# Kernel optimization log

Measured on AMD Instinct MI355X. Metric: run time of the kernel, lower is better.

Reference implementation:

```python
import jax, jax.numpy as jnp
import numpy as np

N = 600000          # points
V = 120000          # occupied voxels (60k per sample)
BEV_H = 512
BEV_W = 512
B = 2
BN_EPS = 1e-3


def setup_inputs() -> dict:
    key = jax.random.key(0)
    k1, k2, k3, k4, k5 = jax.random.split(key, 5)
    bev_coordinate = jax.random.normal(k1, (N, 3), jnp.float32) * 20.0
    bev_local_coordinate = jax.random.normal(k2, (N, 3), jnp.float32)
    intensity = jax.random.uniform(k3, (N,), jnp.float32)
    bev_mapping_pv = jax.random.randint(k4, (N,), 0, V, jnp.int32)
    # unique (batch, h, w) per voxel: 60k voxels/sample spread over 512*512 grid
    v = np.arange(V)
    per_batch = V // B
    flat = (v % per_batch) * (BEV_H * BEV_W // per_batch)  # stride 4, unique
    bev_mapping_vf = jnp.asarray(
        np.stack([v // per_batch, flat // BEV_W, flat % BEV_W], axis=1),
        dtype=jnp.int32)
    W = jax.random.normal(k5, (64, 10), jnp.float32) * (1.0 / np.sqrt(10))
    gamma = jnp.ones((64,), jnp.float32)
    beta = jnp.zeros((64,), jnp.float32)
    return {
        "bev_coordinate": bev_coordinate,
        "bev_local_coordinate": bev_local_coordinate,
        "intensity": intensity,
        "bev_mapping_pv": bev_mapping_pv,
        "bev_mapping_vf": bev_mapping_vf,
        "W": W,
        "gamma": gamma,
        "beta": beta,
        "batch_size": B,
    }


def reference(bev_coordinate, bev_local_coordinate, intensity,
              bev_mapping_pv, bev_mapping_vf, W, gamma, beta, batch_size):
    nvox = bev_mapping_vf.shape[0]
    pv = bev_mapping_pv
    # scatterMean: per-voxel mean of coordinates, gathered back per point
    counts = jnp.zeros((nvox,), bev_coordinate.dtype).at[pv].add(1.0)
    sums = jnp.zeros((nvox, 3), bev_coordinate.dtype).at[pv].add(bev_coordinate)
    vox_mean = sums / jnp.maximum(counts, 1.0)[:, None]
    point_mean = vox_mean[pv]                              # [N,3]
    # feature: [coord(3), intensity(1), coord-mean(3), local(3)] -> [N,10]
    feature = jnp.concatenate(
        [bev_coordinate, intensity[:, None],
         bev_coordinate - point_mean, bev_local_coordinate], axis=1)
    # Linear(10,64,bias=False) + BatchNorm1d(train mode, batch stats) + ReLU
    x = feature @ W.T                                      # [N,64]
    mu = jnp.mean(x, axis=0)
    var = jnp.mean(jnp.square(x - mu), axis=0)             # biased, as torch BN
    x = (x - mu) * jax.lax.rsqrt(var + BN_EPS) * gamma + beta
    x = jax.nn.relu(x)
    # scatterMax into voxels, empty voxels stay at finfo.min (as torch impl)
    vox_max = jnp.full((nvox, 64), jnp.finfo(x.dtype).min, x.dtype).at[pv].max(x)
    # dense scatter_nd into [B,H,W,64], then channels_first
    dense = jnp.zeros((batch_size, BEV_H, BEV_W, 64), x.dtype)
    dense = dense.at[bev_mapping_vf[:, 0], bev_mapping_vf[:, 1],
                     bev_mapping_vf[:, 2]].set(vox_max)
    return jnp.transpose(dense, (0, 3, 1, 2))              # [B,64,H,W]
```

## Files before the change

### kernel.cpp

```cpp
#include <hip/hip_runtime.h>
#include <float.h>

#define EMPTY_FILL (-3.3895313892515355e38f)

#define HW 262144
#define BEVW 512
#define NBPM 256



__global__ void k_init(int* counts, int V, int* inv, int ncell) {
    int i = blockIdx.x * blockDim.x + threadIdx.x;
    int st = gridDim.x * blockDim.x;
    for (int t = i; t < V; t += st) counts[t] = 0;
    for (int t = i; t < ncell; t += st) inv[t] = -1;
}

__global__ void k_count(const int* __restrict__ pv, int n, int* __restrict__ counts) {
    int i = blockIdx.x * blockDim.x + threadIdx.x;
    if (i < n) atomicAdd(&counts[pv[i]], 1);
}

__global__ void k_scan1(const int* __restrict__ counts, int V, int* __restrict__ partials) {
    __shared__ int sh[256];
    int base = blockIdx.x * 2048;
    int s = 0;
    for (int e = 0; e < 8; ++e) {
        int idx = base + e * 256 + threadIdx.x;
        if (idx < V) s += counts[idx];
    }
    sh[threadIdx.x] = s; __syncthreads();
    for (int d = 128; d > 0; d >>= 1) {
        if (threadIdx.x < d) sh[threadIdx.x] += sh[threadIdx.x + d];
        __syncthreads();
    }
    if (threadIdx.x == 0) partials[blockIdx.x] = sh[0];
}

__global__ void k_scan2(const int* __restrict__ partials, int NB, int* __restrict__ blockoff) {
    __shared__ int sh[256];
    int run = 0;
    for (int base = 0; base < NB; base += 256) {
        int idx = base + threadIdx.x;
        int p = (idx < NB) ? partials[idx] : 0;
        __syncthreads();
        sh[threadIdx.x] = p; __syncthreads();
        for (int d = 1; d < 256; d <<= 1) {
            int v2 = sh[threadIdx.x];
            if (threadIdx.x >= d) v2 += sh[threadIdx.x - d];
            __syncthreads(); sh[threadIdx.x] = v2; __syncthreads();
        }
        if (idx < NB) blockoff[idx] = run + sh[threadIdx.x] - p;
        run += sh[255];
    }
}

__global__ void k_scan3(const int* __restrict__ counts, int V,
                        const int* __restrict__ blockoff, int* __restrict__ cursor) {
    __shared__ int sh[256];
    int t = threadIdx.x;
    int base = blockIdx.x * 2048 + t * 8;
    int c[8]; int s = 0;
#pragma unroll
    for (int e = 0; e < 8; ++e) {
        int idx = base + e;
        c[e] = (idx < V) ? counts[idx] : 0;
        s += c[e];
    }
    sh[t] = s; __syncthreads();
    for (int d = 1; d < 256; d <<= 1) {
        int v2 = sh[t];
        if (t >= d) v2 += sh[t - d];
        __syncthreads(); sh[t] = v2; __syncthreads();
    }
    int run = blockoff[blockIdx.x] + sh[t] - s;
#pragma unroll
    for (int e = 0; e < 8; ++e) {
        int idx = base + e;
        if (idx < V) cursor[idx] = run;
        run += c[e];
    }
}

__global__ void k_fill(const int* __restrict__ pv,
                       const float* __restrict__ coord,
                       const float* __restrict__ locc,
                       const float* __restrict__ inten, int n,
                       int* __restrict__ cursor,
                       float4* __restrict__ pdata) {
    int i = blockIdx.x * blockDim.x + threadIdx.x;
    if (i >= n) return;
    int pos = atomicAdd(&cursor[pv[i]], 1);
    pdata[2*pos]   = make_float4(coord[3*i], coord[3*i+1], coord[3*i+2], inten[i]);
    pdata[2*pos+1] = make_float4(locc[3*i],  locc[3*i+1],  locc[3*i+2],  0.f);
}

__global__ void k_pmoments(const float* __restrict__ coord,
                           const float* __restrict__ locc,
                           const float* __restrict__ inten, int n,
                           float* __restrict__ parts) {
    __shared__ float sm[35];
    if (threadIdx.x < 35) sm[threadIdx.x] = 0.f;
    __syncthreads();
    float acc[35];
#pragma unroll
    for (int t = 0; t < 35; ++t) acc[t] = 0.f;
    int i = blockIdx.x * blockDim.x + threadIdx.x;
    int st = gridDim.x * blockDim.x;
    for (; i < n; i += st) {
        float r[7];
        r[0] = coord[3*i]; r[1] = coord[3*i+1]; r[2] = coord[3*i+2];
        r[3] = inten[i];
        r[4] = locc[3*i]; r[5] = locc[3*i+1]; r[6] = locc[3*i+2];
        int t = 0;
#pragma unroll
        for (int j = 0; j < 7; ++j)
#pragma unroll
            for (int k = j; k < 7; ++k) { acc[t] += r[j]*r[k]; ++t; }
#pragma unroll
        for (int j = 0; j < 7; ++j) acc[28+j] += r[j];
    }
#pragma unroll
    for (int t = 0; t < 35; ++t) {
        float x = acc[t];
#pragma unroll
        for (int m = 1; m < 64; m <<= 1) x += __shfl_xor(x, m, 64);
        acc[t] = x;
    }
    if ((threadIdx.x & 63) == 0) {
#pragma unroll
        for (int t = 0; t < 35; ++t) atomicAdd(&sm[t], acc[t]);
    }
    __syncthreads();
    if (threadIdx.x < 35) parts[blockIdx.x * 35 + threadIdx.x] = sm[threadIdx.x];
}

__global__ void k_voxstat(const float4* __restrict__ pdata,
                          const int* __restrict__ counts,
                          const int* __restrict__ cursor, int V,
                          float* __restrict__ vmean,
                          float* __restrict__ parts) {
    __shared__ float sm[18];
    if (threadIdx.x < 18) sm[threadIdx.x] = 0.f;
    __syncthreads();
    int v = blockIdx.x * blockDim.x + threadIdx.x;
    float acc[18];
#pragma unroll
    for (int t = 0; t < 18; ++t) acc[t] = 0.f;
    if (v < V) {
        int cnt = counts[v];
        int end = cursor[v];
        int st = end - cnt;
        float s0=0.f,s1=0.f,s2=0.f,si=0.f,l0=0.f,l1=0.f,l2=0.f;
        for (int k = st; k < end; ++k) {
            float4 a = pdata[2*k];
            float4 b = pdata[2*k+1];
            s0 += a.x; s1 += a.y; s2 += a.z; si += a.w;
            l0 += b.x; l1 += b.y; l2 += b.z;
        }
        float inv_ = 1.f / fmaxf((float)cnt, 1.f);
        float m0 = s0*inv_, m1 = s1*inv_, m2 = s2*inv_;
        vmean[3*v] = m0; vmean[3*v+1] = m1; vmean[3*v+2] = m2;
        float cf = (float)cnt;
        acc[0]=cf*m0*m0; acc[1]=cf*m0*m1; acc[2]=cf*m0*m2;
        acc[3]=cf*m1*m1; acc[4]=cf*m1*m2; acc[5]=cf*m2*m2;
        acc[6]=m0*si; acc[7]=m1*si; acc[8]=m2*si;
        acc[9]=m0*l0;  acc[10]=m0*l1; acc[11]=m0*l2;
        acc[12]=m1*l0; acc[13]=m1*l1; acc[14]=m1*l2;
        acc[15]=m2*l0; acc[16]=m2*l1; acc[17]=m2*l2;
    }
#pragma unroll
    for (int t = 0; t < 18; ++t) {
        float x = acc[t];
#pragma unroll
        for (int m = 1; m < 64; m <<= 1) x += __shfl_xor(x, m, 64);
        acc[t] = x;
    }
    if ((threadIdx.x & 63) == 0) {
#pragma unroll
        for (int t = 0; t < 18; ++t) atomicAdd(&sm[t], acc[t]);
    }
    __syncthreads();
    if (threadIdx.x < 18) parts[blockIdx.x * 18 + threadIdx.x] = sm[threadIdx.x];
}

__global__ void k_bn_final(const float* __restrict__ pm, int nbpm,
                           const float* __restrict__ pvs, int nbvs,
                           const float* __restrict__ W,
                           const float* __restrict__ gamma,
                           const float* __restrict__ beta,
                           int n, float* __restrict__ ss) {
    __shared__ double red[53][16];
    __shared__ double g[53];
    __shared__ double MF[10][10];
    __shared__ double SF[10];
    int tid = threadIdx.x;
    int t16 = tid >> 4;
    int l16 = tid & 15;
    double s = 0.0;
    if (t16 < 35) {
        for (int b = l16; b < nbpm; b += 16) s += (double)pm[b * 35 + t16];
        red[t16][l16] = s;
    } else if (t16 < 53) {
        int u = t16 - 35;
        for (int b = l16; b < nbvs; b += 16) s += (double)pvs[b * 18 + u];
        red[t16][l16] = s;
    }
    __syncthreads();
    if (tid < 53) {
        double a = 0.0;
#pragma unroll
        for (int k = 0; k < 16; ++k) a += red[tid][k];
        g[tid] = a;
    }
    __syncthreads();
    if (tid == 0) {
        double M7[7][7], S7[7], Pmm[3][3], Qmi[3], Rml[3][3];
        int t = 0;
        for (int j = 0; j < 7; ++j)
            for (int k = j; k < 7; ++k) { M7[j][k] = M7[k][j] = g[t]; ++t; }
        for (int j = 0; j < 7; ++j) S7[j] = g[28+j];
        t = 35;
        for (int j = 0; j < 3; ++j)
            for (int k = j; k < 3; ++k) { Pmm[j][k] = Pmm[k][j] = g[t]; ++t; }
        for (int k = 0; k < 3; ++k) Qmi[k] = g[41+k];
        for (int j = 0; j < 3; ++j)
            for (int k = 0; k < 3; ++k) Rml[j][k] = g[44+3*j+k];
        const int rmap[10] = {0,1,2,3,-1,-1,-1,4,5,6};
        for (int a = 0; a < 10; ++a)
            for (int b = a; b < 10; ++b) {
                bool ad = (a >= 4 && a < 7), bd = (b >= 4 && b < 7);
                double val;
                if (!ad && !bd) val = M7[rmap[a]][rmap[b]];
                else if (ad && bd) val = M7[a-4][b-4] - Pmm[a-4][b-4];
                else {
                    int k = ad ? a-4 : b-4;
                    int o = ad ? b : a;
                    int ro = rmap[o];
                    double X;
                    if (o < 3) X = Pmm[o][k];
                    else if (o == 3) X = Qmi[k];
                    else X = Rml[k][ro-4];
                    val = M7[ro][k] - X;
                }
                MF[a][b] = MF[b][a] = val;
            }
        for (int a = 0; a < 10; ++a)
            SF[a] = (a >= 4 && a < 7) ? 0.0 : S7[rmap[a]];
    }
    __syncthreads();
    int c = tid;
    if (c >= 64) return;
    double w[10];
    for (int j = 0; j < 10; ++j) w[j] = (double)W[c*10+j];
    double invn = 1.0 / (double)n;
    double mu = 0.0;
    for (int j = 0; j < 10; ++j) mu += w[j] * SF[j] * invn;
    double ex2 = 0.0;
    for (int j = 0; j < 10; ++j) {
        double sj = 0.0;
        for (int k = 0; k < 10; ++k) sj += MF[j][k] * w[k];
        ex2 += w[j] * sj;
    }
    ex2 *= invn;
    double var = ex2 - mu*mu;
    double scale = (double)gamma[c] / sqrt(var + 1e-3);
    double shift = (double)beta[c] - mu*scale;
    ss[c] = (float)scale;
    ss[64+c] = (float)shift;
}

__global__ void k_vox(const float4* __restrict__ pdata,
                      const int* __restrict__ counts,
                      const int* __restrict__ cursor,
                      const float* __restrict__ vmean,
                      const int* __restrict__ vf, int V,
                      const float* __restrict__ W,
                      const float* __restrict__ ss,
                      float* __restrict__ vfeat,
                      int* __restrict__ inv) {
    const int lane = threadIdx.x & 63;
    const int wave = blockIdx.x * (blockDim.x >> 6) + (threadIdx.x >> 6);
    const int nw = gridDim.x * (blockDim.x >> 6);
    const int vpw = (V + nw - 1) / nw;
    const int v0 = wave * vpw;
    if (v0 >= V) return;
    const int v1 = (v0 + vpw < V) ? (v0 + vpw) : V;
    float wr[10];
#pragma unroll
    for (int j = 0; j < 10; ++j) wr[j] = W[lane*10 + j];
    const float scale = ss[lane];
    const float shift = ss[64 + lane];
    const float su0 = (wr[0]+wr[4])*scale, su1 = (wr[1]+wr[5])*scale,
                su2 = (wr[2]+wr[6])*scale, sw3 = wr[3]*scale,
                sw7 = wr[7]*scale, sw8 = wr[8]*scale, sw9 = wr[9]*scale,
                sv0 = wr[4]*scale, sv1 = wr[5]*scale, sv2 = wr[6]*scale;
    for (int v = v0; v < v1; ++v) {
        const int cnt = counts[v];
        const int end = cursor[v];
        float m;
        if (cnt == 0) {
            m = EMPTY_FILL;
        } else {
            const float off = shift - (sv0*vmean[3*v] + sv1*vmean[3*v+1]
                                       + sv2*vmean[3*v+2]);
            float mm = -FLT_MAX;
#pragma unroll 2
            for (int k = end - cnt; k < end; ++k) {
                float4 a = pdata[2*k];
                float4 b = pdata[2*k+1];
                float y = su0*a.x + su1*a.y + su2*a.z + sw3*a.w
                        + sw7*b.x + sw8*b.y + sw9*b.z;
                mm = fmaxf(mm, y);
            }
            m = fmaxf(mm + off, 0.f);
        }
        vfeat[(size_t)v*64 + lane] = m;
        if (lane == 0) {
            inv[vf[3*v]*HW + vf[3*v+1]*BEVW + vf[3*v+2]] = v;
        }
    }
}

__global__ void k_out(const float* __restrict__ vfeat,
                      const int* __restrict__ inv,
                      int ncell, float* __restrict__ out) {
    int cell = blockIdx.x * blockDim.x + threadIdx.x;
    if (cell >= ncell) return;
    int v = inv[cell];
    int b = cell >> 18;
    int hw = cell & (HW - 1);
    float* ob = out + ((size_t)b << 24) + hw;
    const float4* vb = (const float4*)(vfeat + (size_t)(v >= 0 ? v : 0) * 64);
#pragma unroll
    for (int c0 = 0; c0 < 16; ++c0) {
        float4 q = (v >= 0) ? vb[c0] : make_float4(0.f, 0.f, 0.f, 0.f);
        ob[(size_t)(4*c0+0) * HW] = q.x;
        ob[(size_t)(4*c0+1) * HW] = q.y;
        ob[(size_t)(4*c0+2) * HW] = q.z;
        ob[(size_t)(4*c0+3) * HW] = q.w;
    }
}


__global__ void k_zero4(float4* a, long na, float4* b, long nb) {
    long i = (long)blockIdx.x * blockDim.x + threadIdx.x;
    long st = (long)gridDim.x * blockDim.x;
    float4 z = make_float4(0.f, 0.f, 0.f, 0.f);
    for (long t = i; t < na; t += st) a[t] = z;
    for (long t = i; t < nb; t += st) b[t] = z;
}

__global__ void k_scatter_mean7(const float* __restrict__ coord,
                                const float* __restrict__ locc,
                                const float* __restrict__ inten,
                                const int* __restrict__ pv, int n,
                                float* __restrict__ countsf,
                                float* __restrict__ sums7) {
    int i = blockIdx.x * blockDim.x + threadIdx.x;
    if (i >= n) return;
    int v = pv[i];
    atomicAdd(&countsf[v], 1.0f);
    atomicAdd(&sums7[7*v+0], coord[3*i+0]);
    atomicAdd(&sums7[7*v+1], coord[3*i+1]);
    atomicAdd(&sums7[7*v+2], coord[3*i+2]);
    atomicAdd(&sums7[7*v+3], inten[i]);
    atomicAdd(&sums7[7*v+4], locc[3*i+0]);
    atomicAdd(&sums7[7*v+5], locc[3*i+1]);
    atomicAdd(&sums7[7*v+6], locc[3*i+2]);
}

__global__ void k_vstat_fb(const float* __restrict__ countsf,
                           const float* __restrict__ sums7, int V,
                           float* __restrict__ vmean, float* __restrict__ parts) {
    __shared__ float sm[18];
    if (threadIdx.x < 18) sm[threadIdx.x] = 0.f;
    __syncthreads();
    int v = blockIdx.x * blockDim.x + threadIdx.x;
    float acc[18];
#pragma unroll
    for (int t = 0; t < 18; ++t) acc[t] = 0.f;
    if (v < V) {
        float cf = countsf[v];
        float inv_ = 1.f / fmaxf(cf, 1.f);
        float m0 = sums7[7*v]*inv_, m1 = sums7[7*v+1]*inv_, m2 = sums7[7*v+2]*inv_;
        float si = sums7[7*v+3], l0 = sums7[7*v+4], l1 = sums7[7*v+5], l2 = sums7[7*v+6];
        vmean[3*v] = m0; vmean[3*v+1] = m1; vmean[3*v+2] = m2;
        acc[0]=cf*m0*m0; acc[1]=cf*m0*m1; acc[2]=cf*m0*m2;
        acc[3]=cf*m1*m1; acc[4]=cf*m1*m2; acc[5]=cf*m2*m2;
        acc[6]=m0*si; acc[7]=m1*si; acc[8]=m2*si;
        acc[9]=m0*l0;  acc[10]=m0*l1; acc[11]=m0*l2;
        acc[12]=m1*l0; acc[13]=m1*l1; acc[14]=m1*l2;
        acc[15]=m2*l0; acc[16]=m2*l1; acc[17]=m2*l2;
    }
#pragma unroll
    for (int t = 0; t < 18; ++t) {
        float x = acc[t];
#pragma unroll
        for (int m = 1; m < 64; m <<= 1) x += __shfl_xor(x, m, 64);
        acc[t] = x;
    }
    if ((threadIdx.x & 63) == 0) {
#pragma unroll
        for (int t = 0; t < 18; ++t) atomicAdd(&sm[t], acc[t]);
    }
    __syncthreads();
    if (threadIdx.x < 18) parts[blockIdx.x * 18 + threadIdx.x] = sm[threadIdx.x];
}

__global__ void k_scatter_max_dense(const float* __restrict__ coord,
                                    const float* __restrict__ locc,
                                    const float* __restrict__ inten,
                                    const int* __restrict__ pv, int n,
                                    const float* __restrict__ vmean,
                                    const float* __restrict__ W,
                                    const float* __restrict__ ss,
                                    const int* __restrict__ vf,
                                    unsigned int* __restrict__ outbits) {
    const int lane = threadIdx.x & 63;
    const int wave = blockIdx.x * (blockDim.x >> 6) + (threadIdx.x >> 6);
    const int nwaves = gridDim.x * (blockDim.x >> 6);
    float wr[10];
#pragma unroll
    for (int j = 0; j < 10; ++j) wr[j] = W[lane*10 + j];
    const float scale = ss[lane];
    const float shift = ss[64 + lane];
    const int cpw = (n + nwaves - 1) / nwaves;
    const int p0 = wave * cpw;
    const int p1 = (p0 + cpw < n) ? (p0 + cpw) : n;
    for (int p = p0; p < p1; ++p) {
        int v = pv[p];
        float c0 = coord[3*p], c1 = coord[3*p+1], c2 = coord[3*p+2];
        float x = wr[0]*c0 + wr[1]*c1 + wr[2]*c2 + wr[3]*inten[p]
                + wr[4]*(c0-vmean[3*v]) + wr[5]*(c1-vmean[3*v+1]) + wr[6]*(c2-vmean[3*v+2])
                + wr[7]*locc[3*p] + wr[8]*locc[3*p+1] + wr[9]*locc[3*p+2];
        float y = fmaxf(x*scale + shift, 0.0f);
        int b = vf[3*v], h = vf[3*v+1], w = vf[3*v+2];
        size_t idx = (((size_t)b*64 + lane)*BEVW + h)*BEVW + w;
        atomicMax(&outbits[idx], __float_as_uint(y));
    }
}

__global__ void k_fix_empty_dense(const float* __restrict__ countsf,
                                  const int* __restrict__ vf, int V,
                                  float* __restrict__ out) {
    int v = blockIdx.x * blockDim.x + threadIdx.x;
    if (v >= V) return;
    if (countsf[v] > 0.f) return;
    int b = vf[3*v], h = vf[3*v+1], w = vf[3*v+2];
    for (int c = 0; c < 64; ++c)
        out[(((size_t)b*64 + c)*BEVW + h)*BEVW + w] = EMPTY_FILL;
}


static inline size_t rup(size_t x) { return (x + 255) & ~(size_t)255; }

extern "C" void kernel_launch(void* const* d_in, const int* in_sizes, int n_in,
                              void* d_out, int out_size, void* d_ws, size_t ws_size,
                              hipStream_t stream) {
    const float* coord = (const float*)d_in[0];
    const float* locc  = (const float*)d_in[1];
    const float* inten = (const float*)d_in[2];
    const int*   pv    = (const int*)d_in[3];
    const int*   vf    = (const int*)d_in[4];
    const float* W     = (const float*)d_in[5];
    const float* gamma = (const float*)d_in[6];
    const float* beta  = (const float*)d_in[7];
    const int n = in_sizes[2];
    const int V = in_sizes[4] / 3;
    const int B = out_size / (64 * HW);
    const int ncell = B * HW;
    const int NB = (V + 2047) / 2048;
    const int vxblk = (V + 255) / 256;
    const int ptblk = (n + 255) / 256;

    char* ws = (char*)d_ws;
    size_t off = 0;
    int*   counts   = (int*)(ws + off);   off = rup(off + (size_t)V * 4);
    int*   cursor   = (int*)(ws + off);   off = rup(off + (size_t)V * 4);
    int*   partials = (int*)(ws + off);   off = rup(off + (size_t)NB * 4);
    int*   blockoff = (int*)(ws + off);   off = rup(off + (size_t)NB * 4);
    float* parts_pm = (float*)(ws + off); off = rup(off + (size_t)NBPM * 35 * 4);
    float* parts_vs = (float*)(ws + off); off = rup(off + (size_t)vxblk * 18 * 4);
    float* ss       = (float*)(ws + off); off = rup(off + 512);
    float* vmean    = (float*)(ws + off); off = rup(off + (size_t)V * 12);
    int*   inv      = (int*)(ws + off);   off = rup(off + (size_t)ncell * 4);
    float* vfeat    = (float*)(ws + off); off = rup(off + (size_t)V * 256);
    bool big = (ws_size >= off) && ((size_t)out_size * 4 >= (size_t)n * 32);

    float4* pdata = (float4*)d_out;

    if (big) {
        k_init<<<2048, 256, 0, stream>>>(counts, V, inv, ncell);
        k_count<<<ptblk, 256, 0, stream>>>(pv, n, counts);
        k_scan1<<<NB, 256, 0, stream>>>(counts, V, partials);
        k_scan2<<<1, 256, 0, stream>>>(partials, NB, blockoff);
        k_scan3<<<NB, 256, 0, stream>>>(counts, V, blockoff, cursor);
        k_fill<<<ptblk, 256, 0, stream>>>(pv, coord, locc, inten, n, cursor, pdata);
        k_pmoments<<<NBPM, 256, 0, stream>>>(coord, locc, inten, n, parts_pm);
        k_voxstat<<<vxblk, 256, 0, stream>>>(pdata, counts, cursor, V, vmean, parts_vs);
        k_bn_final<<<1, 1024, 0, stream>>>(parts_pm, NBPM, parts_vs, vxblk,
                                           W, gamma, beta, n, ss);
        k_vox<<<2048, 256, 0, stream>>>(pdata, counts, cursor, vmean,
                                        vf, V, W, ss, vfeat, inv);
        k_out<<<(ncell + 255) / 256, 256, 0, stream>>>(vfeat, inv, ncell, (float*)d_out);
    } else {
        size_t o2 = 0;
        float* countsf  = (float*)(ws + o2); o2 = rup(o2 + (size_t)V * 4);
        float* sums7b   = (float*)(ws + o2); o2 = rup(o2 + (size_t)V * 28);
        float* parts_p2 = (float*)(ws + o2); o2 = rup(o2 + (size_t)NBPM * 35 * 4);
        float* parts_v2 = (float*)(ws + o2); o2 = rup(o2 + (size_t)vxblk * 18 * 4);
        float* ss2      = (float*)(ws + o2); o2 = rup(o2 + 512);
        float* vmean2   = (float*)(ws + o2); o2 = rup(o2 + (size_t)V * 12);
        k_zero4<<<2048, 256, 0, stream>>>((float4*)ws, (long)(o2 / 16),
                                          (float4*)d_out, (long)out_size / 4);
        k_scatter_mean7<<<ptblk, 256, 0, stream>>>(coord, locc, inten, pv, n,
                                                   countsf, sums7b);
        k_pmoments<<<NBPM, 256, 0, stream>>>(coord, locc, inten, n, parts_p2);
        k_vstat_fb<<<vxblk, 256, 0, stream>>>(countsf, sums7b, V, vmean2, parts_v2);
        k_bn_final<<<1, 1024, 0, stream>>>(parts_p2, NBPM, parts_v2, vxblk,
                                           W, gamma, beta, n, ss2);
        k_scatter_max_dense<<<2048, 256, 0, stream>>>(coord, locc, inten, pv, n,
                                                      vmean2, W, ss2, vf,
                                                      (unsigned int*)d_out);
        k_fix_empty_dense<<<vxblk, 256, 0, stream>>>(countsf, vf, V, (float*)d_out);
    }
}
```

Measured before the change: 199.9 us.

## Fuse scan kernels, merge point moments into fill, use nontemporal output stores

Drops the single-block k_scan2 by having each k_scan3 block reduce the partials before it, and folds the per-point moment accumulation into the fill kernel so the point data is read once. The output scatter now uses nontemporal stores, and the init kernel launches fewer blocks. This removes two launches and one full pass over the point inputs. In exchange, k_bn_final has to reduce ptblk partial moment sets instead of NBPM, and the fill kernel carries 35 accumulators per thread.

```diff
diff --git a/kernel.cpp b/kernel.cpp
--- a/kernel.cpp
+++ b/kernel.cpp
@@ -37,28 +37,22 @@
     if (threadIdx.x == 0) partials[blockIdx.x] = sh[0];
 }
 
-__global__ void k_scan2(const int* __restrict__ partials, int NB, int* __restrict__ blockoff) {
+__global__ void k_scan3(const int* __restrict__ counts, int V,
+                        const int* __restrict__ partials,
+                        int* __restrict__ cursor) {
     __shared__ int sh[256];
-    int run = 0;
-    for (int base = 0; base < NB; base += 256) {
-        int idx = base + threadIdx.x;
-        int p = (idx < NB) ? partials[idx] : 0;
+    __shared__ int boff;
+    int t = threadIdx.x;
+    int s0 = 0;
+    for (int b = t; b < blockIdx.x; b += 256) s0 += partials[b];
+    sh[t] = s0; __syncthreads();
+    for (int d = 128; d > 0; d >>= 1) {
+        if (t < d) sh[t] += sh[t + d];
         __syncthreads();
-        sh[threadIdx.x] = p; __syncthreads();
-        for (int d = 1; d < 256; d <<= 1) {
-            int v2 = sh[threadIdx.x];
-            if (threadIdx.x >= d) v2 += sh[threadIdx.x - d];
-            __syncthreads(); sh[threadIdx.x] = v2; __syncthreads();
-        }
-        if (idx < NB) blockoff[idx] = run + sh[threadIdx.x] - p;
-        run += sh[255];
-    }
-}
-
-__global__ void k_scan3(const int* __restrict__ counts, int V,
-                        const int* __restrict__ blockoff, int* __restrict__ cursor) {
-    __shared__ int sh[256];
-    int t = threadIdx.x;
+    }
+    if (t == 0) boff = sh[0];
+    __syncthreads();
+
     int base = blockIdx.x * 2048 + t * 8;
     int c[8]; int s = 0;
 #pragma unroll
@@ -67,13 +61,14 @@
         c[e] = (idx < V) ? counts[idx] : 0;
         s += c[e];
     }
+    __syncthreads();
     sh[t] = s; __syncthreads();
     for (int d = 1; d < 256; d <<= 1) {
         int v2 = sh[t];
         if (t >= d) v2 += sh[t - d];
         __syncthreads(); sh[t] = v2; __syncthreads();
     }
-    int run = blockoff[blockIdx.x] + sh[t] - s;
+    int run = boff + sh[t] - s;
 #pragma unroll
     for (int e = 0; e < 8; ++e) {
         int idx = base + e;
@@ -82,17 +77,50 @@
     }
 }
 
-__global__ void k_fill(const int* __restrict__ pv,
-                       const float* __restrict__ coord,
-                       const float* __restrict__ locc,
-                       const float* __restrict__ inten, int n,
-                       int* __restrict__ cursor,
-                       float4* __restrict__ pdata) {
-    int i = blockIdx.x * blockDim.x + threadIdx.x;
-    if (i >= n) return;
-    int pos = atomicAdd(&cursor[pv[i]], 1);
-    pdata[2*pos]   = make_float4(coord[3*i], coord[3*i+1], coord[3*i+2], inten[i]);
-    pdata[2*pos+1] = make_float4(locc[3*i],  locc[3*i+1],  locc[3*i+2],  0.f);
+__global__ void k_fillm(const int* __restrict__ pv,
+                        const float* __restrict__ coord,
+                        const float* __restrict__ locc,
+                        const float* __restrict__ inten, int n,
+                        int* __restrict__ cursor,
+                        float4* __restrict__ pdata,
+                        float* __restrict__ parts) {
+    __shared__ float sm[35];
+    if (threadIdx.x < 35) sm[threadIdx.x] = 0.f;
+    __syncthreads();
+    float acc[35];
+#pragma unroll
+    for (int t = 0; t < 35; ++t) acc[t] = 0.f;
+    int stride = gridDim.x * blockDim.x;
+    for (int i = blockIdx.x * blockDim.x + threadIdx.x; i < n; i += stride) {
+        int v = pv[i];
+        float r[7];
+        r[0] = coord[3*i]; r[1] = coord[3*i+1]; r[2] = coord[3*i+2];
+        r[3] = inten[i];
+        r[4] = locc[3*i]; r[5] = locc[3*i+1]; r[6] = locc[3*i+2];
+        int pos = atomicAdd(&cursor[v], 1);
+        pdata[2*pos]   = make_float4(r[0], r[1], r[2], r[3]);
+        pdata[2*pos+1] = make_float4(r[4], r[5], r[6], 0.f);
+        int t = 0;
+#pragma unroll
+        for (int j = 0; j < 7; ++j)
+#pragma unroll
+            for (int k = j; k < 7; ++k) { acc[t] += r[j]*r[k]; ++t; }
+#pragma unroll
+        for (int j = 0; j < 7; ++j) acc[28+j] += r[j];
+    }
+#pragma unroll
+    for (int t = 0; t < 35; ++t) {
+        float x = acc[t];
+#pragma unroll
+        for (int m = 1; m < 64; m <<= 1) x += __shfl_xor(x, m, 64);
+        acc[t] = x;
+    }
+    if ((threadIdx.x & 63) == 0) {
+#pragma unroll
+        for (int t = 0; t < 35; ++t) atomicAdd(&sm[t], acc[t]);
+    }
+    __syncthreads();
+    if (threadIdx.x < 35) parts[blockIdx.x * 35 + threadIdx.x] = sm[threadIdx.x];
 }
 
 __global__ void k_pmoments(const float* __restrict__ coord,
@@ -335,10 +363,10 @@
 #pragma unroll
     for (int c0 = 0; c0 < 16; ++c0) {
         float4 q = (v >= 0) ? vb[c0] : make_float4(0.f, 0.f, 0.f, 0.f);
-        ob[(size_t)(4*c0+0) * HW] = q.x;
-        ob[(size_t)(4*c0+1) * HW] = q.y;
-        ob[(size_t)(4*c0+2) * HW] = q.z;
-        ob[(size_t)(4*c0+3) * HW] = q.w;
+        __builtin_nontemporal_store(q.x, &ob[(size_t)(4*c0+0) * HW]);
+        __builtin_nontemporal_store(q.y, &ob[(size_t)(4*c0+1) * HW]);
+        __builtin_nontemporal_store(q.z, &ob[(size_t)(4*c0+2) * HW]);
+        __builtin_nontemporal_store(q.w, &ob[(size_t)(4*c0+3) * HW]);
     }
 }
 
@@ -479,8 +507,7 @@
     int*   counts   = (int*)(ws + off);   off = rup(off + (size_t)V * 4);
     int*   cursor   = (int*)(ws + off);   off = rup(off + (size_t)V * 4);
     int*   partials = (int*)(ws + off);   off = rup(off + (size_t)NB * 4);
-    int*   blockoff = (int*)(ws + off);   off = rup(off + (size_t)NB * 4);
-    float* parts_pm = (float*)(ws + off); off = rup(off + (size_t)NBPM * 35 * 4);
+    float* parts_pm = (float*)(ws + off); off = rup(off + (size_t)ptblk * 35 * 4);
     float* parts_vs = (float*)(ws + off); off = rup(off + (size_t)vxblk * 18 * 4);
     float* ss       = (float*)(ws + off); off = rup(off + 512);
     float* vmean    = (float*)(ws + off); off = rup(off + (size_t)V * 12);
@@ -491,15 +518,14 @@
     float4* pdata = (float4*)d_out;
 
     if (big) {
-        k_init<<<2048, 256, 0, stream>>>(counts, V, inv, ncell);
+        k_init<<<512, 256, 0, stream>>>(counts, V, inv, ncell);
         k_count<<<ptblk, 256, 0, stream>>>(pv, n, counts);
         k_scan1<<<NB, 256, 0, stream>>>(counts, V, partials);
-        k_scan2<<<1, 256, 0, stream>>>(partials, NB, blockoff);
-        k_scan3<<<NB, 256, 0, stream>>>(counts, V, blockoff, cursor);
-        k_fill<<<ptblk, 256, 0, stream>>>(pv, coord, locc, inten, n, cursor, pdata);
-        k_pmoments<<<NBPM, 256, 0, stream>>>(coord, locc, inten, n, parts_pm);
+        k_scan3<<<NB, 256, 0, stream>>>(counts, V, partials, cursor);
+        k_fillm<<<ptblk, 256, 0, stream>>>(pv, coord, locc, inten, n, cursor,
+                                           pdata, parts_pm);
         k_voxstat<<<vxblk, 256, 0, stream>>>(pdata, counts, cursor, V, vmean, parts_vs);
-        k_bn_final<<<1, 1024, 0, stream>>>(parts_pm, NBPM, parts_vs, vxblk,
+        k_bn_final<<<1, 1024, 0, stream>>>(parts_pm, ptblk, parts_vs, vxblk,
                                            W, gamma, beta, n, ss);
         k_vox<<<2048, 256, 0, stream>>>(pdata, counts, cursor, vmean,
                                         vf, V, W, ss, vfeat, inv);
```

After: 260.0 us. 1.3x slower.
